# Performance work log

Measured on AMD Instinct MI355X. Metric: run time of the kernel, lower is better.

## Reference

```python
import jax, jax.numpy as jnp
import numpy as np
from jax import lax

EPS = 1e-5
N_CROPS = 501
CROP_W = 500
RF = 65          # temporal receptive field
KS = 15          # conv1 kernel size
POOL = 3


def _bn(x, g, b, m, v, axis=1):
    shp = [1] * x.ndim
    shp[axis] = -1
    inv = g.reshape(shp) / jnp.sqrt(v.reshape(shp) + EPS)
    return (x - m.reshape(shp)) * inv + b.reshape(shp)


def setup_inputs() -> dict:
    key = jax.random.key(0)
    ks = jax.random.split(key, 16)
    B, C_IN, CH, T = 16, 1, 22, 1001
    F = 36
    OUT = 4
    FLAT = F * 43  # 1548 (corrected fc in_features; repo constant 504 is inconsistent)
    d = {
        "x": jax.random.normal(ks[0], (B, C_IN, CH, T), jnp.float32),
        # temporal conv [1,65]
        "w_t": jax.random.normal(ks[1], (F, 1, 1, RF), jnp.float32) * 0.1,
        "b_t": jax.random.normal(ks[2], (F,), jnp.float32) * 0.1,
        "bn_t_g": jax.random.uniform(ks[3], (F,), jnp.float32, 0.5, 1.5),
        "bn_t_b": jax.random.normal(ks[4], (F,), jnp.float32) * 0.1,
        "bn_t_m": jax.random.normal(ks[5], (F,), jnp.float32) * 0.1,
        "bn_t_v": jax.random.uniform(ks[6], (F,), jnp.float32, 0.5, 1.5),
        # spatial conv [22,1]
        "w_s": jax.random.normal(ks[7], (F, F, CH, 1), jnp.float32) * 0.05,
        "b_s": jax.random.normal(ks[8], (F,), jnp.float32) * 0.1,
        "bn_s_g": jax.random.uniform(ks[9], (F,), jnp.float32, 0.5, 1.5),
        "bn_s_b": jax.random.normal(ks[10], (F,), jnp.float32) * 0.1,
        "bn_s_m": jax.random.normal(ks[11], (F,), jnp.float32) * 0.1,
        "bn_s_v": jax.random.uniform(ks[12], (F,), jnp.float32, 0.5, 1.5),
        # conv1 [1,15] (as 1-D conv over time)
        "w_c": jax.random.normal(ks[13], (F, F, KS), jnp.float32) * 0.05,
        "b_c": jax.random.normal(ks[14], (F,), jnp.float32) * 0.1,
        "bn_c_g": jnp.ones((F,), jnp.float32),
        "bn_c_b": jnp.zeros((F,), jnp.float32),
        "bn_c_m": jnp.zeros((F,), jnp.float32),
        "bn_c_v": jnp.ones((F,), jnp.float32),
        # fc
        "w_fc": jax.random.normal(ks[15], (OUT, FLAT), jnp.float32) * 0.02,
        "b_fc": jnp.zeros((OUT,), jnp.float32),
    }
    return d


def reference(x, w_t, b_t, bn_t_g, bn_t_b, bn_t_m, bn_t_v,
              w_s, b_s, bn_s_g, bn_s_b, bn_s_m, bn_s_v,
              w_c, b_c, bn_c_g, bn_c_b, bn_c_m, bn_c_v,
              w_fc, b_fc):
    B = x.shape[0]
    F = w_t.shape[0]
    OUT = b_fc.shape[0]

    # temporal + spatial conv/BN/ELU are shift-invariant -> compute once over full T
    h = lax.conv_general_dilated(x, w_t, (1, 1), 'VALID',
                                 dimension_numbers=('NCHW', 'OIHW', 'NCHW'))
    h = h + b_t[None, :, None, None]                       # [B,36,22,937]
    h = jax.nn.elu(_bn(h, bn_t_g, bn_t_b, bn_t_m, bn_t_v))
    h = lax.conv_general_dilated(h, w_s, (1, 1), 'VALID',
                                 dimension_numbers=('NCHW', 'OIHW', 'NCHW'))
    h = h + b_s[None, :, None, None]                       # [B,36,1,937]
    h = jax.nn.elu(_bn(h, bn_s_g, bn_s_b, bn_s_m, bn_s_v))
    h = h[:, :, 0, :]                                      # [B,36,937]

    TW = CROP_W - RF + 1  # 436: temporal width of each crop after temporal conv

    def crop_logits(i):
        sl = lax.dynamic_slice_in_dim(h, i, TW, axis=2)    # [B,36,436]
        p1 = sl[:, :, :435].reshape(B, F, 145, POOL).mean(-1)  # avgpool1 -> [B,36,145]
        c = lax.conv_general_dilated(p1, w_c, (1,), 'VALID',
                                     dimension_numbers=('NCH', 'OIH', 'NCH'))
        c = c + b_c[None, :, None]                          # [B,36,131]
        c = jax.nn.elu(_bn(c, bn_c_g, bn_c_b, bn_c_m, bn_c_v))
        p2 = c[:, :, :129].reshape(B, F, 43, POOL).mean(-1)  # avgpool2 -> [B,36,43]
        flat = p2.reshape(B, -1)                            # [B,1548]
        return flat @ w_fc.T + b_fc                         # [B,OUT]

    def step(acc, i):
        return acc + crop_logits(i), None

    init = jnp.zeros((B, OUT), x.dtype)
    total, _ = lax.scan(step, init, jnp.arange(N_CROPS))
    return total / N_CROPS
```

## Files before the change

kernel.cpp:

```cpp
#include <hip/hip_runtime.h>

#define EPS 1e-5f
#define B 16
#define CH 22
#define CH2 24
#define T_IN 1001
#define F 36
#define RF 65
#define T1 937
#define UN 885
#define PSP 944
#define KS 15
#define GN 295
#define WN 129
#define M43 43
#define BF 576
#define FLAT 1548
#define NZ 8

#define P_OFF   0
#define A_OFF   543744
#define H2P_OFF 1053504
#define WTT_OFF 5366880
#define WST_OFF 5369220
#define WCQ_OFF 5400324
#define BN_OFF  5426244

__device__ __forceinline__ float elu_f(float v) {
    return v > 0.f ? v : (__expf(v) - 1.f);
}

__global__ __launch_bounds__(256) void k_prep(
    const float* __restrict__ w_t, const float* __restrict__ w_s,
    const float* __restrict__ w_c,
    const float* __restrict__ b_t, const float* __restrict__ g_t,
    const float* __restrict__ be_t,const float* __restrict__ m_t,
    const float* __restrict__ v_t,
    const float* __restrict__ b_s, const float* __restrict__ g_s,
    const float* __restrict__ be_s,const float* __restrict__ m_s,
    const float* __restrict__ v_s,
    const float* __restrict__ b_c, const float* __restrict__ g_c,
    const float* __restrict__ be_c,const float* __restrict__ m_c,
    const float* __restrict__ v_c, const float* __restrict__ b_fc,
    float* __restrict__ wtT, float* __restrict__ wsTp,
    float* __restrict__ wcQ, float* __restrict__ bnz,
    float* __restrict__ out)
{
    int i = blockIdx.x * 256 + threadIdx.x;
    if (i < F * RF)     { int k = i / F,  fi = i % F; wtT[i] = w_t[fi * RF + k]; }
    if (i < F * CH2 * F) {
        int fi = i / (CH2 * F);
        int r  = i % (CH2 * F);
        int ch = r / F, fo = r % F;
        wsTp[i] = (ch < CH) ? w_s[(fo * F + fi) * CH + ch] : 0.f;
    }
    if (i < 12 * 36 * 15 * 4) {
        int t3 = i / (36 * 15 * 4);
        int r  = i % (36 * 15 * 4);
        int f  = r / 60;
        int r2 = r % 60;
        int k  = r2 / 4, j = r2 % 4;
        wcQ[i] = (j < 3) ? w_c[((3 * t3 + j) * F + f) * KS + k] : 0.f;
    }
    if (i < F) {
        float s1 = g_t[i] * rsqrtf(v_t[i] + EPS);
        bnz[i]          = s1;
        bnz[F + i]      = (b_t[i] - m_t[i]) * s1 + be_t[i];
        float s2 = g_s[i] * rsqrtf(v_s[i] + EPS);
        bnz[2 * F + i]  = s2;
        bnz[3 * F + i]  = (b_s[i] - m_s[i]) * s2 + be_s[i];
        float s3 = g_c[i] * rsqrtf(v_c[i] + EPS);
        bnz[4 * F + i]  = s3;
        bnz[5 * F + i]  = (b_c[i] - m_c[i]) * s3 + be_c[i];
    }
    if (i < B * 4) out[i] = b_fc[i & 3];
}

__global__ __launch_bounds__(256) void k_fused(
    const float* __restrict__ x, const float* __restrict__ wtT,
    const float* __restrict__ wsTp, const float* __restrict__ bnz,
    float* __restrict__ h2p)
{
    __shared__ float xs[3 * 128];
    __shared__ float comb[2][64][F];
    const int tid  = threadIdx.x;
    const int lane = tid & 63;
    const int w = __builtin_amdgcn_readfirstlane(tid >> 6);
    const int b  = blockIdx.y;
    const int z  = blockIdx.z;
    const int t0 = blockIdx.x * 64;
    const int ch0 = z * 3;
    const int fi0 = w * 9;

    for (int i = tid; i < 3 * 128; i += 256) {
        int c = i >> 7, j = i & 127;
        int ch = ch0 + c;
        int t = t0 + j; if (t > T_IN - 1) t = T_IN - 1;
        xs[i] = (ch < CH) ? x[(b * CH + ch) * T_IN + t] : 0.f;
    }
    __syncthreads();

    float acc[F];
    #pragma unroll
    for (int fo = 0; fo < F; ++fo) acc[fo] = 0.f;

    for (int c = 0; c < 3; ++c) {
        const float* xr = xs + c * 128 + lane;

        float h1a[9];
        #pragma unroll
        for (int j = 0; j < 9; ++j) h1a[j] = 0.f;

        #pragma unroll 8
        for (int kp = 0; kp < 32; ++kp) {
            const int k = 2 * kp;
            float xv0 = xr[k];
            float xv1 = xr[k + 1];
            const float* w0 = wtT + k * F + fi0;
            const float* w1 = w0 + F;
            #pragma unroll
            for (int j = 0; j < 9; ++j) {
                h1a[j] += xv0 * w0[j];
                h1a[j] += xv1 * w1[j];
            }
        }
        {
            float xv = xr[64];
            const float* w64 = wtT + 64 * F + fi0;
            #pragma unroll
            for (int j = 0; j < 9; ++j) h1a[j] += xv * w64[j];
        }

        #pragma unroll
        for (int j = 0; j < 9; ++j)
            h1a[j] = elu_f(h1a[j] * bnz[fi0 + j] + bnz[F + fi0 + j]);

        #pragma unroll
        for (int j = 0; j < 9; ++j) {
            const float* wr = wsTp + ((fi0 + j) * CH2 + ch0 + c) * F;
            float e = h1a[j];
            #pragma unroll
            for (int fo = 0; fo < F; ++fo)
                acc[fo] += e * wr[fo];
        }
    }

    if (w >= 2) {
        float4* cb = (float4*)&comb[w - 2][lane][0];
        #pragma unroll
        for (int j = 0; j < 9; ++j)
            cb[j] = make_float4(acc[4*j], acc[4*j+1], acc[4*j+2], acc[4*j+3]);
    }
    __syncthreads();
    if (w < 2) {
        const float4* cb = (const float4*)&comb[w][lane][0];
        #pragma unroll
        for (int j = 0; j < 9; ++j) {
            float4 v = cb[j];
            acc[4*j]   += v.x; acc[4*j+1] += v.y;
            acc[4*j+2] += v.z; acc[4*j+3] += v.w;
        }
    }
    __syncthreads();
    if (w == 1) {
        float4* cb = (float4*)&comb[0][lane][0];
        #pragma unroll
        for (int j = 0; j < 9; ++j)
            cb[j] = make_float4(acc[4*j], acc[4*j+1], acc[4*j+2], acc[4*j+3]);
    }
    __syncthreads();
    if (w == 0) {
        const float4* cb = (const float4*)&comb[0][lane][0];
        #pragma unroll
        for (int j = 0; j < 9; ++j) {
            float4 v = cb[j];
            acc[4*j]   += v.x; acc[4*j+1] += v.y;
            acc[4*j+2] += v.z; acc[4*j+3] += v.w;
        }
        int t = t0 + lane;
        if (t < T1) {
            #pragma unroll
            for (int fo = 0; fo < F; ++fo)
                h2p[((size_t)(z * BF + b * F + fo)) * T1 + t] = acc[fo];
        }
    }
}

__global__ __launch_bounds__(256) void k_hpool(
    const float* __restrict__ h2p, const float* __restrict__ bnz,
    float* __restrict__ P)
{
    __shared__ float Ls[T1];
    const int bf = blockIdx.x;
    const int f = bf % F;
    const float s2 = bnz[2 * F + f], o2 = bnz[3 * F + f];
    for (int i = threadIdx.x; i < T1; i += 256) {
        float s = 0.f;
        #pragma unroll
        for (int z = 0; z < NZ; ++z)
            s += h2p[((size_t)(z * BF + bf)) * T1 + i];
        Ls[i] = elu_f(s * s2 + o2);
    }
    __syncthreads();
    float* Pr = P + (size_t)bf * PSP;
    for (int i = threadIdx.x; i < PSP; i += 256) {
        int s0 = i     < T1 - 1 ? i     : T1 - 1;
        int s1 = i + 1 < T1 - 1 ? i + 1 : T1 - 1;
        int s2i= i + 2 < T1 - 1 ? i + 2 : T1 - 1;
        Pr[i] = (Ls[s0] + Ls[s1] + Ls[s2i]) * (1.f / 3.f);
    }
}

__global__ __launch_bounds__(768) void k_qconv(
    const float* __restrict__ P, const float* __restrict__ wcQ,
    const float* __restrict__ bnz, float* __restrict__ A)
{
    const int tid  = threadIdx.x;
    const int lane = tid & 63;
    const int t3 = __builtin_amdgcn_readfirstlane(tid >> 6);
    const int b  = blockIdx.y;
    const int u0 = blockIdx.x * 64;
    const int fo0 = t3 * 3;

    const float* wq = wcQ + t3 * (36 * 60);

    float a0 = 0.f, a1 = 0.f, a2 = 0.f;

    for (int f = 0; f < F; ++f) {
        const float* Pr = P + (size_t)(b * F + f) * PSP + u0 + lane;
        const float* wf = wq + f * 60;
        #pragma unroll
        for (int k = 0; k < KS; ++k) {
            float pv = Pr[3 * k];
            a0 += pv * wf[4 * k + 0];
            a1 += pv * wf[4 * k + 1];
            a2 += pv * wf[4 * k + 2];
        }
    }

    int u = u0 + lane;
    if (u < UN) {
        float sc0 = bnz[4 * F + fo0 + 0], oc0 = bnz[5 * F + fo0 + 0];
        float sc1 = bnz[4 * F + fo0 + 1], oc1 = bnz[5 * F + fo0 + 1];
        float sc2 = bnz[4 * F + fo0 + 2], oc2 = bnz[5 * F + fo0 + 2];
        A[((size_t)(b * F + fo0 + 0)) * UN + u] = elu_f(a0 * sc0 + oc0);
        A[((size_t)(b * F + fo0 + 1)) * UN + u] = elu_f(a1 * sc1 + oc1);
        A[((size_t)(b * F + fo0 + 2)) * UN + u] = elu_f(a2 * sc2 + oc2);
    }
}

__global__ __launch_bounds__(256) void k_wins(
    const float* __restrict__ A, const float* __restrict__ w_fc,
    float* __restrict__ out)
{
    __shared__ float Es[UN];
    __shared__ float G[GN];
    __shared__ float Ws[WN];
    __shared__ float Sm[M43];
    const int tid = threadIdx.x;
    const int bf = blockIdx.x;
    const int b = bf / F, f = bf % F;
    for (int i = tid; i < UN; i += 256)
        Es[i] = A[(size_t)bf * UN + i];
    __syncthreads();
    for (int q = tid; q < GN; q += 256)
        G[q] = Es[3 * q] + Es[3 * q + 1] + Es[3 * q + 2];
    __syncthreads();
    if (tid < WN) {
        float a = 0.f;
        for (int q = tid; q < tid + 167; ++q) a += G[q];
        Ws[tid] = a;
    }
    __syncthreads();
    if (tid < M43)
        Sm[tid] = (Ws[3 * tid] + Ws[3 * tid + 1] + Ws[3 * tid + 2]) * (1.f / 3.f);
    __syncthreads();
    if (tid < 4) {
        const float* wr = w_fc + tid * FLAT + f * M43;
        float a = 0.f;
        #pragma unroll 43
        for (int m = 0; m < M43; ++m) a += Sm[m] * wr[m];
        atomicAdd(&out[b * 4 + tid], a * (1.f / 501.f));
    }
}

extern "C" void kernel_launch(void* const* d_in, const int* in_sizes, int n_in,
                              void* d_out, int out_size, void* d_ws, size_t ws_size,
                              hipStream_t stream) {
    const float* x    = (const float*)d_in[0];
    const float* w_t  = (const float*)d_in[1];
    const float* b_t  = (const float*)d_in[2];
    const float* g_t  = (const float*)d_in[3];
    const float* be_t = (const float*)d_in[4];
    const float* m_t  = (const float*)d_in[5];
    const float* v_t  = (const float*)d_in[6];
    const float* w_s  = (const float*)d_in[7];
    const float* b_s  = (const float*)d_in[8];
    const float* g_s  = (const float*)d_in[9];
    const float* be_s = (const float*)d_in[10];
    const float* m_s  = (const float*)d_in[11];
    const float* v_s  = (const float*)d_in[12];
    const float* w_c  = (const float*)d_in[13];
    const float* b_c  = (const float*)d_in[14];
    const float* g_c  = (const float*)d_in[15];
    const float* be_c = (const float*)d_in[16];
    const float* m_c  = (const float*)d_in[17];
    const float* v_c  = (const float*)d_in[18];
    const float* w_fc = (const float*)d_in[19];
    const float* b_fc = (const float*)d_in[20];

    float* ws   = (float*)d_ws;
    float* P    = ws + P_OFF;
    float* A    = ws + A_OFF;
    float* h2p  = ws + H2P_OFF;
    float* wtT  = ws + WTT_OFF;
    float* wsTp = ws + WST_OFF;
    float* wcQ  = ws + WCQ_OFF;
    float* bnz  = ws + BN_OFF;
    float* out  = (float*)d_out;

    k_prep<<<dim3(128), 256, 0, stream>>>(
        w_t, w_s, w_c, b_t, g_t, be_t, m_t, v_t,
        b_s, g_s, be_s, m_s, v_s, b_c, g_c, be_c, m_c, v_c, b_fc,
        wtT, wsTp, wcQ, bnz, out);

    k_fused<<<dim3(15, B, NZ), 256, 0, stream>>>(x, wtT, wsTp, bnz, h2p);
    k_hpool<<<dim3(BF), 256, 0, stream>>>(h2p, bnz, P);
    k_qconv<<<dim3(14, B), 768, 0, stream>>>(P, wcQ, bnz, A);
    k_wins<<<dim3(BF), 256, 0, stream>>>(A, w_fc, out);
}
```

Baseline: 201.6 us.

## Reorder fused conv loops to share weight loads across channels and regroup weights

The temporal-conv loop now handles all three input channels inside one k loop, so each temporal weight load is reused three times instead of being reloaded per channel. The temporal and spatial weights are repacked in the prep kernel into per-wave, per-z contiguous blocks padded to 12/24-wide groups for aligned, vectorizable scalar loads. A launch bound of 4 blocks per CU is added. The cost is more live registers (27 accumulators on top of 36), which could cause spills under the tighter register limit.

```diff
diff --git a/kernel.cpp b/kernel.cpp
--- a/kernel.cpp
+++ b/kernel.cpp
@@ -21,10 +21,10 @@
 #define P_OFF   0
 #define A_OFF   543744
 #define H2P_OFF 1053504
-#define WTT_OFF 5366880
-#define WST_OFF 5369220
-#define WCQ_OFF 5400324
-#define BN_OFF  5426244
+#define WTG_OFF 5366880
+#define WSG_OFF 5370048
+#define WCQ_OFF 5401152
+#define BN_OFF  5427072
 
 __device__ __forceinline__ float elu_f(float v) {
     return v > 0.f ? v : (__expf(v) - 1.f);
@@ -42,17 +42,28 @@
     const float* __restrict__ b_c, const float* __restrict__ g_c,
     const float* __restrict__ be_c,const float* __restrict__ m_c,
     const float* __restrict__ v_c, const float* __restrict__ b_fc,
-    float* __restrict__ wtT, float* __restrict__ wsTp,
+    float* __restrict__ wtG, float* __restrict__ wsG,
     float* __restrict__ wcQ, float* __restrict__ bnz,
     float* __restrict__ out)
 {
     int i = blockIdx.x * 256 + threadIdx.x;
-    if (i < F * RF)     { int k = i / F,  fi = i % F; wtT[i] = w_t[fi * RF + k]; }
-    if (i < F * CH2 * F) {
-        int fi = i / (CH2 * F);
-        int r  = i % (CH2 * F);
-        int ch = r / F, fo = r % F;
-        wsTp[i] = (ch < CH) ? w_s[(fo * F + fi) * CH + ch] : 0.f;
+    if (i < 4 * 33 * 24) {
+        int g  = i / (33 * 24);
+        int r  = i % (33 * 24);
+        int kp = r / 24, slot = r % 24;
+        int kk = slot / 12, j = slot % 12;
+        int k  = 2 * kp + kk;
+        wtG[i] = (j < 9 && k < RF) ? w_t[(g * 9 + j) * RF + k] : 0.f;
+    }
+    if (i < 4 * 8 * 27 * 36) {
+        int g  = i / (8 * 27 * 36);
+        int r  = i % (8 * 27 * 36);
+        int z  = r / (27 * 36);
+        int r2 = r % (27 * 36);
+        int jc = r2 / 36, fo = r2 % 36;
+        int j  = jc / 3, c = jc % 3;
+        int fi = g * 9 + j, ch = z * 3 + c;
+        wsG[i] = (ch < CH) ? w_s[(fo * F + fi) * CH + ch] : 0.f;
     }
     if (i < 12 * 36 * 15 * 4) {
         int t3 = i / (36 * 15 * 4);
@@ -76,9 +87,9 @@
     if (i < B * 4) out[i] = b_fc[i & 3];
 }
 
-__global__ __launch_bounds__(256) void k_fused(
-    const float* __restrict__ x, const float* __restrict__ wtT,
-    const float* __restrict__ wsTp, const float* __restrict__ bnz,
+__global__ __launch_bounds__(256, 4) void k_fused(
+    const float* __restrict__ x, const float* __restrict__ wtG,
+    const float* __restrict__ wsG, const float* __restrict__ bnz,
     float* __restrict__ h2p)
 {
     __shared__ float xs[3 * 128];
@@ -100,45 +111,55 @@
     }
     __syncthreads();
 
+    const float* wgB = wtG + w * (33 * 24);
+
+    float h1a[3][9];
+    #pragma unroll
+    for (int c = 0; c < 3; ++c)
+        #pragma unroll
+        for (int j = 0; j < 9; ++j) h1a[c][j] = 0.f;
+
+    #pragma unroll 8
+    for (int kp = 0; kp < 32; ++kp) {
+        const float* wp = wgB + kp * 24;
+        #pragma unroll
+        for (int c = 0; c < 3; ++c) {
+            float xv0 = xs[c * 128 + lane + 2 * kp];
+            float xv1 = xs[c * 128 + lane + 2 * kp + 1];
+            #pragma unroll
+            for (int j = 0; j < 9; ++j)
+                h1a[c][j] += xv0 * wp[j] + xv1 * wp[12 + j];
+        }
+    }
+    {
+        const float* wp = wgB + 32 * 24;
+        #pragma unroll
+        for (int c = 0; c < 3; ++c) {
+            float xv = xs[c * 128 + lane + 64];
+            #pragma unroll
+            for (int j = 0; j < 9; ++j) h1a[c][j] += xv * wp[j];
+        }
+    }
+
+    #pragma unroll
+    for (int j = 0; j < 9; ++j) {
+        float s1 = bnz[fi0 + j], o1 = bnz[F + fi0 + j];
+        #pragma unroll
+        for (int c = 0; c < 3; ++c)
+            h1a[c][j] = elu_f(h1a[c][j] * s1 + o1);
+    }
+
     float acc[F];
     #pragma unroll
     for (int fo = 0; fo < F; ++fo) acc[fo] = 0.f;
 
-    for (int c = 0; c < 3; ++c) {
-        const float* xr = xs + c * 128 + lane;
-
-        float h1a[9];
-        #pragma unroll
-        for (int j = 0; j < 9; ++j) h1a[j] = 0.f;
-
-        #pragma unroll 8
-        for (int kp = 0; kp < 32; ++kp) {
-            const int k = 2 * kp;
-            float xv0 = xr[k];
-            float xv1 = xr[k + 1];
-            const float* w0 = wtT + k * F + fi0;
-            const float* w1 = w0 + F;
-            #pragma unroll
-            for (int j = 0; j < 9; ++j) {
-                h1a[j] += xv0 * w0[j];
-                h1a[j] += xv1 * w1[j];
-            }
-        }
-        {
-            float xv = xr[64];
-            const float* w64 = wtT + 64 * F + fi0;
-            #pragma unroll
-            for (int j = 0; j < 9; ++j) h1a[j] += xv * w64[j];
-        }
-
-        #pragma unroll
-        for (int j = 0; j < 9; ++j)
-            h1a[j] = elu_f(h1a[j] * bnz[fi0 + j] + bnz[F + fi0 + j]);
-
-        #pragma unroll
-        for (int j = 0; j < 9; ++j) {
-            const float* wr = wsTp + ((fi0 + j) * CH2 + ch0 + c) * F;
-            float e = h1a[j];
+    const float* wsB = wsG + (w * NZ + z) * (27 * 36);
+    #pragma unroll
+    for (int j = 0; j < 9; ++j) {
+        #pragma unroll
+        for (int c = 0; c < 3; ++c) {
+            const float* wr = wsB + (j * 3 + c) * 36;
+            float e = h1a[c][j];
             #pragma unroll
             for (int fo = 0; fo < F; ++fo)
                 acc[fo] += e * wr[fo];
@@ -313,8 +334,8 @@
     float* P    = ws + P_OFF;
     float* A    = ws + A_OFF;
     float* h2p  = ws + H2P_OFF;
-    float* wtT  = ws + WTT_OFF;
-    float* wsTp = ws + WST_OFF;
+    float* wtG  = ws + WTG_OFF;
+    float* wsG  = ws + WSG_OFF;
     float* wcQ  = ws + WCQ_OFF;
     float* bnz  = ws + BN_OFF;
     float* out  = (float*)d_out;
@@ -322,9 +343,9 @@
     k_prep<<<dim3(128), 256, 0, stream>>>(
         w_t, w_s, w_c, b_t, g_t, be_t, m_t, v_t,
         b_s, g_s, be_s, m_s, v_s, b_c, g_c, be_c, m_c, v_c, b_fc,
-        wtT, wsTp, wcQ, bnz, out);
-
-    k_fused<<<dim3(15, B, NZ), 256, 0, stream>>>(x, wtT, wsTp, bnz, h2p);
+        wtG, wsG, wcQ, bnz, out);
+
+    k_fused<<<dim3(15, B, NZ), 256, 0, stream>>>(x, wtG, wsG, bnz, h2p);
     k_hpool<<<dim3(BF), 256, 0, stream>>>(h2p, bnz, P);
     k_qconv<<<dim3(14, B), 768, 0, stream>>>(P, wcQ, bnz, A);
     k_wins<<<dim3(BF), 256, 0, stream>>>(A, w_fc, out);
```

Result: faster. 197.0 us (-2.3%).
